# Optimization experiments

Hardware: AMD Instinct MI355X
Metric: run time of the kernel (lower is better)

## Reference

```python
import jax, jax.numpy as jnp
import numpy as np

N, L = 1, 384
NODE, H, PD = 256, 8, 128
HD = NODE // H
D1 = H * PD + NODE  # out_transform input dim = 1280


def instance_norm(x, eps=1e-5):
    # x: (N, C, H, W); torch InstanceNorm2d default: no affine, biased var
    m = x.mean(axis=(2, 3), keepdims=True)
    v = x.var(axis=(2, 3), keepdims=True)
    return (x - m) / jnp.sqrt(v + eps)


def conv3x3(x, w, b):
    y = jax.lax.conv_general_dilated(x, w, (1, 1), 'SAME',
                                     dimension_numbers=('NCHW', 'OIHW', 'NCHW'))
    return y + b[None, :, None, None]


def leaky(x):
    return jnp.where(x >= 0, x, 0.01 * x)


def layer_norm(x, w, b, eps=1e-5):
    m = x.mean(-1, keepdims=True)
    v = x.var(-1, keepdims=True)
    return (x - m) / jnp.sqrt(v + eps) * w + b


def setup_inputs() -> dict:
    key = jax.random.key(0)
    ks = jax.random.split(key, 32)
    s = 0.05
    inp = {
        'x': jax.random.normal(ks[0], (N, L, NODE), jnp.float32),
        'z': jax.random.normal(ks[1], (N, L, L, PD), jnp.float32),
        'plddt': jax.random.uniform(ks[2], (N, L, L, 1), jnp.float32),
        # linear weights stored (in, out) so application is x @ W
        'Wq': jax.random.normal(ks[3], (NODE, NODE), jnp.float32) * s,
        'Wk': jax.random.normal(ks[4], (NODE, NODE), jnp.float32) * s,
        'Wv': jax.random.normal(ks[5], (NODE, NODE), jnp.float32) * s,
        'Wp2a': jax.random.normal(ks[6], (PD, H), jnp.float32) * s,
        'conv_a_w': jax.random.normal(ks[7], (H, 2 * H, 3, 3), jnp.float32) * s,
        'conv_a_b': jnp.zeros((H,), jnp.float32),
        'conv_m_w': jax.random.normal(ks[8], (H, H + 1, 3, 3), jnp.float32) * s,
        'conv_m_b': jnp.zeros((H,), jnp.float32),
        'ln1_w': jnp.ones((D1,), jnp.float32),
        'ln1_b': jnp.zeros((D1,), jnp.float32),
        'lin1_w': jax.random.normal(ks[9], (D1, 2 * NODE), jnp.float32) * s,
        'lin1_b': jnp.zeros((2 * NODE,), jnp.float32),
        'ln2_w': jnp.ones((2 * NODE,), jnp.float32),
        'ln2_b': jnp.zeros((2 * NODE,), jnp.float32),
        'lin2_w': jax.random.normal(ks[10], (2 * NODE, NODE), jnp.float32) * s,
        'lin2_b': jnp.zeros((NODE,), jnp.float32),
        'lnf_w': jnp.ones((NODE,), jnp.float32),
        'lnf_b': jnp.zeros((NODE,), jnp.float32),
        'conv_p_w': jax.random.normal(ks[11], (PD, H + PD, 3, 3), jnp.float32) * s,
        'conv_p_b': jnp.zeros((PD,), jnp.float32),
    }
    return inp


def reference(x, z, plddt, Wq, Wk, Wv, Wp2a, conv_a_w, conv_a_b, conv_m_w,
              conv_m_b, ln1_w, ln1_b, lin1_w, lin1_b, ln2_w, ln2_b, lin2_w,
              lin2_b, lnf_w, lnf_b, conv_p_w, conv_p_b):
    Nb, Lh, D = x.shape
    nh = conv_a_w.shape[0]
    hd = D // nh
    Pd = z.shape[-1]
    # node -> alpha (GAT-style QK scores per head)
    q = (x @ Wq).reshape(Nb, Lh, nh, hd)
    k = (x @ Wk).reshape(Nb, Lh, nh, hd)
    v = (x @ Wv).reshape(Nb, Lh, nh, hd)
    a_node = jnp.einsum('nlhd,nmhd->nlmh', q, k) / jnp.sqrt(jnp.float32(hd))
    a_pair = z @ Wp2a                                  # (N,L,L,H)
    a = jnp.concatenate([a_pair, a_node], -1).transpose(0, 3, 1, 2)  # (N,2H,L,L)
    a = leaky(conv3x3(instance_norm(a), conv_a_w, conv_a_b))
    a = jnp.concatenate([a, plddt.transpose(0, 3, 1, 2)], 1)          # (N,H+1,L,L)
    a = leaky(conv3x3(instance_norm(a), conv_m_w, conv_m_b))
    a = a.transpose(0, 2, 3, 1)                                        # (N,L,L,H)
    # aggregations
    nfn = jnp.einsum('nlmh,nmhd->nlhd', a, v).reshape(Nb, Lh, D)       # node from node
    nfp = jnp.einsum('nlmh,nlmp->nlhp', a, z).reshape(Nb, Lh, nh * Pd) # node from pair
    cat = jnp.concatenate([nfp, nfn], -1)
    h = layer_norm(cat, ln1_w, ln1_b) @ lin1_w + lin1_b
    h = leaky(layer_norm(h, ln2_w, ln2_b)) @ lin2_w + lin2_b
    x_new = layer_norm(x + h, lnf_w, lnf_b)
    zp = jnp.concatenate([z, a], -1).transpose(0, 3, 1, 2)             # (N,P+H,L,L)
    z_new = leaky(conv3x3(instance_norm(zp), conv_p_w, conv_p_b)).transpose(0, 2, 3, 1)
    return x_new, z_new
```

## Files before the change

kernel.cpp:

```cpp
#include <hip/hip_runtime.h>
#include <stdint.h>

#define LSEQ 384
#define LL   147456
#define NODE 256
#define NH   8
#define HD   32
#define PDIM 128
#define D1   1280
#define D2   512

typedef __attribute__((ext_vector_type(8))) short s16x8;
typedef __attribute__((ext_vector_type(8))) __bf16 bf16x8;
typedef __attribute__((ext_vector_type(4))) float f32x4;

__device__ __forceinline__ float bf2f(uint16_t u) {
    union { uint32_t i; float f; } x; x.i = ((uint32_t)u) << 16; return x.f;
}
__device__ __forceinline__ uint16_t f2bf(float f) {
    uint32_t b = __float_as_uint(f);
    return (uint16_t)((b + 0x7FFFu + ((b >> 16) & 1u)) >> 16);
}
__device__ __forceinline__ float ld(const void* p, size_t i, int bf) {
    return bf ? bf2f(((const uint16_t*)p)[i]) : ((const float*)p)[i];
}
__device__ __forceinline__ void stout(void* p, size_t i, float v, int bf) {
    if (bf) ((uint16_t*)p)[i] = f2bf(v);
    else    ((float*)p)[i] = v;
}

__device__ __forceinline__ bf16x8 bf16x8_zero() {
    union { s16x8 s; bf16x8 b; } u; u.s = (s16x8)0; return u.b;
}

__device__ __forceinline__ void block_reduce2_256(float* s1, float* s2, int t) {
    __syncthreads();
    for (int o = 128; o > 0; o >>= 1) {
        if (t < o) { s1[t] += s1[t + o]; s2[t] += s2[t + o]; }
        __syncthreads();
    }
}

__device__ __forceinline__ void acc8(uint4 u, float& s, float& ss) {
    uint32_t w[4] = { u.x, u.y, u.z, u.w };
    #pragma unroll
    for (int i = 0; i < 4; ++i) {
        float a = bf2f((uint16_t)(w[i] & 0xFFFFu));
        float b = bf2f((uint16_t)(w[i] >> 16));
        s += a + b;
        ss = fmaf(a, a, ss);
        ss = fmaf(b, b, ss);
    }
}

__global__ void k_detect(const uint32_t* __restrict__ zz, int* __restrict__ flag) {
    if (threadIdx.x == 0 && blockIdx.x == 0) {
        int cnt = 0;
        for (int i = 0; i < 256; ++i) {
            uint32_t lo = zz[i] & 0xFFFFu;
            uint32_t e = (lo >> 7) & 0xFFu;
            if (lo == 0u || (e >= 96u && e <= 142u)) ++cnt;
        }
        flag[0] = (cnt >= 192) ? 1 : 0;
    }
}

__global__ __launch_bounds__(256) void k_cvt(
    const void* __restrict__ src, uint16_t* __restrict__ dst, const int* __restrict__ dt)
{
    int bf = dt[0];
    int i = blockIdx.x * 256 + threadIdx.x;
    dst[i] = f2bf(ld(src, i, bf));
}

__global__ __launch_bounds__(256) void k_wnk(
    const void* __restrict__ src, uint16_t* __restrict__ dst, int K, int N,
    const int* __restrict__ dt)
{
    int bf = dt[0];
    int n = blockIdx.x;
    for (int e = threadIdx.x; e < K; e += 256)
        dst[(size_t)n * K + e] = f2bf(ld(src, (size_t)e * N + n, bf));
}

__global__ __launch_bounds__(256) void k_gemm_bias_f32(
    const uint16_t* __restrict__ A, const uint16_t* __restrict__ B,
    const void* __restrict__ bias, float* __restrict__ out, int K, int N,
    const int* __restrict__ dt)
{
    __shared__ __align__(16) uint16_t As[64 * 72];
    __shared__ __align__(16) uint16_t Bs[64 * 72];
    int bf = dt[0];
    int t = threadIdx.x;
    int row0 = blockIdx.x * 64, col0 = blockIdx.y * 64;
    int w = t >> 6, lane = t & 63, p = lane & 15, g = lane >> 4;
    int wm = w >> 1, wn = w & 1;
    f32x4 acc[2][2];
    #pragma unroll
    for (int i = 0; i < 2; ++i)
        #pragma unroll
        for (int j = 0; j < 2; ++j) acc[i][j] = (f32x4){0.f, 0.f, 0.f, 0.f};

    for (int kc = 0; kc < K; kc += 64) {
        __syncthreads();
        #pragma unroll
        for (int rep = 0; rep < 2; ++rep) {
            int i = t + rep * 256;
            int r = i >> 3, c8 = (i & 7) * 8;
            *(uint4*)&As[r * 72 + c8] = *(const uint4*)&A[(size_t)(row0 + r) * K + kc + c8];
            *(uint4*)&Bs[r * 72 + c8] = *(const uint4*)&B[(size_t)(col0 + r) * K + kc + c8];
        }
        __syncthreads();
        #pragma unroll
        for (int kk = 0; kk < 64; kk += 32) {
            bf16x8 a0 = *(const bf16x8*)&As[(wm * 32 + p) * 72 + kk + 8 * g];
            bf16x8 a1 = *(const bf16x8*)&As[(wm * 32 + 16 + p) * 72 + kk + 8 * g];
            bf16x8 b0 = *(const bf16x8*)&Bs[(wn * 32 + p) * 72 + kk + 8 * g];
            bf16x8 b1 = *(const bf16x8*)&Bs[(wn * 32 + 16 + p) * 72 + kk + 8 * g];
            acc[0][0] = __builtin_amdgcn_mfma_f32_16x16x32_bf16(a0, b0, acc[0][0], 0, 0, 0);
            acc[0][1] = __builtin_amdgcn_mfma_f32_16x16x32_bf16(a0, b1, acc[0][1], 0, 0, 0);
            acc[1][0] = __builtin_amdgcn_mfma_f32_16x16x32_bf16(a1, b0, acc[1][0], 0, 0, 0);
            acc[1][1] = __builtin_amdgcn_mfma_f32_16x16x32_bf16(a1, b1, acc[1][1], 0, 0, 0);
        }
    }
    #pragma unroll
    for (int mi = 0; mi < 2; ++mi)
        #pragma unroll
        for (int ni = 0; ni < 2; ++ni) {
            int n = col0 + wn * 32 + ni * 16 + p;
            float bb = ld(bias, n, bf);
            #pragma unroll
            for (int reg = 0; reg < 4; ++reg) {
                int m = row0 + wm * 32 + mi * 16 + 4 * g + reg;
                out[(size_t)m * N + n] = acc[mi][ni][reg] + bb;
            }
        }
}

__global__ __launch_bounds__(256) void k_gemm_qkv(
    const uint16_t* __restrict__ A, const uint16_t* __restrict__ B,
    uint16_t* __restrict__ q, uint16_t* __restrict__ k, uint16_t* __restrict__ v)
{
    __shared__ __align__(16) uint16_t As[64 * 72];
    __shared__ __align__(16) uint16_t Bs[64 * 72];
    const int K = 256;
    int t = threadIdx.x;
    int row0 = blockIdx.x * 64, col0 = blockIdx.y * 64;
    int w = t >> 6, lane = t & 63, p = lane & 15, g = lane >> 4;
    int wm = w >> 1, wn = w & 1;
    f32x4 acc[2][2];
    #pragma unroll
    for (int i = 0; i < 2; ++i)
        #pragma unroll
        for (int j = 0; j < 2; ++j) acc[i][j] = (f32x4){0.f, 0.f, 0.f, 0.f};

    for (int kc = 0; kc < K; kc += 64) {
        __syncthreads();
        #pragma unroll
        for (int rep = 0; rep < 2; ++rep) {
            int i = t + rep * 256;
            int r = i >> 3, c8 = (i & 7) * 8;
            *(uint4*)&As[r * 72 + c8] = *(const uint4*)&A[(size_t)(row0 + r) * K + kc + c8];
            *(uint4*)&Bs[r * 72 + c8] = *(const uint4*)&B[(size_t)(col0 + r) * K + kc + c8];
        }
        __syncthreads();
        #pragma unroll
        for (int kk = 0; kk < 64; kk += 32) {
            bf16x8 a0 = *(const bf16x8*)&As[(wm * 32 + p) * 72 + kk + 8 * g];
            bf16x8 a1 = *(const bf16x8*)&As[(wm * 32 + 16 + p) * 72 + kk + 8 * g];
            bf16x8 b0 = *(const bf16x8*)&Bs[(wn * 32 + p) * 72 + kk + 8 * g];
            bf16x8 b1 = *(const bf16x8*)&Bs[(wn * 32 + 16 + p) * 72 + kk + 8 * g];
            acc[0][0] = __builtin_amdgcn_mfma_f32_16x16x32_bf16(a0, b0, acc[0][0], 0, 0, 0);
            acc[0][1] = __builtin_amdgcn_mfma_f32_16x16x32_bf16(a0, b1, acc[0][1], 0, 0, 0);
            acc[1][0] = __builtin_amdgcn_mfma_f32_16x16x32_bf16(a1, b0, acc[1][0], 0, 0, 0);
            acc[1][1] = __builtin_amdgcn_mfma_f32_16x16x32_bf16(a1, b1, acc[1][1], 0, 0, 0);
        }
    }
    #pragma unroll
    for (int mi = 0; mi < 2; ++mi)
        #pragma unroll
        for (int ni = 0; ni < 2; ++ni) {
            int nglob = col0 + wn * 32 + ni * 16 + p;
            int sel = nglob >> 8, col = nglob & 255;
            uint16_t* dst = (sel == 0) ? q : (sel == 1) ? k : v;
            #pragma unroll
            for (int reg = 0; reg < 4; ++reg) {
                int m = row0 + wm * 32 + mi * 16 + 4 * g + reg;
                dst[(size_t)m * 256 + col] = f2bf(acc[mi][ni][reg]);
            }
        }
}

__global__ __launch_bounds__(256) void k_lin2lnf_mfma(
    const uint16_t* __restrict__ A, const uint16_t* __restrict__ B,
    const void* __restrict__ bias, const void* __restrict__ x,
    const void* __restrict__ lnw, const void* __restrict__ lnb,
    void* __restrict__ out, const int* __restrict__ dt)
{
    __shared__ __align__(16) uint16_t As[32 * 72];
    __shared__ __align__(16) uint16_t Bs[256 * 72];
    const int K = 512;
    int bf = dt[0];
    int t = threadIdx.x;
    int row0 = blockIdx.x * 32;
    int w = t >> 6, lane = t & 63, p = lane & 15, g = lane >> 4;
    f32x4 acc[2][4];
    #pragma unroll
    for (int i = 0; i < 2; ++i)
        #pragma unroll
        for (int j = 0; j < 4; ++j) acc[i][j] = (f32x4){0.f, 0.f, 0.f, 0.f};

    for (int kc = 0; kc < K; kc += 64) {
        __syncthreads();
        {
            int r = t >> 3, c8 = (t & 7) * 8;
            *(uint4*)&As[r * 72 + c8] = *(const uint4*)&A[(size_t)(row0 + r) * K + kc + c8];
        }
        #pragma unroll
        for (int rep = 0; rep < 8; ++rep) {
            int i = t + rep * 256;
            int r = i >> 3, c8 = (i & 7) * 8;
            *(uint4*)&Bs[r * 72 + c8] = *(const uint4*)&B[(size_t)r * K + kc + c8];
        }
        __syncthreads();
        #pragma unroll
        for (int kk = 0; kk < 64; kk += 32) {
            bf16x8 a0 = *(const bf16x8*)&As[(p) * 72 + kk + 8 * g];
            bf16x8 a1 = *(const bf16x8*)&As[(16 + p) * 72 + kk + 8 * g];
            #pragma unroll
            for (int ni = 0; ni < 4; ++ni) {
                bf16x8 bq = *(const bf16x8*)&Bs[(w * 64 + ni * 16 + p) * 72 + kk + 8 * g];
                acc[0][ni] = __builtin_amdgcn_mfma_f32_16x16x32_bf16(a0, bq, acc[0][ni], 0, 0, 0);
                acc[1][ni] = __builtin_amdgcn_mfma_f32_16x16x32_bf16(a1, bq, acc[1][ni], 0, 0, 0);
            }
        }
    }
    __syncthreads();
    float* lnt = (float*)Bs;
    #pragma unroll
    for (int mi = 0; mi < 2; ++mi)
        #pragma unroll
        for (int ni = 0; ni < 4; ++ni) {
            int n = w * 64 + ni * 16 + p;
            float bb = ld(bias, n, bf);
            #pragma unroll
            for (int reg = 0; reg < 4; ++reg) {
                int m = mi * 16 + 4 * g + reg;
                lnt[m * 264 + n] = acc[mi][ni][reg] + bb + ld(x, (size_t)(row0 + m) * 256 + n, bf);
            }
        }
    __syncthreads();
    for (int rr = 0; rr < 8; ++rr) {
        int m = w * 8 + rr;
        float4 v4 = *(const float4*)&lnt[m * 264 + lane * 4];
        float vv[4] = { v4.x, v4.y, v4.z, v4.w };
        float s = (vv[0] + vv[1]) + (vv[2] + vv[3]);
        float ss = fmaf(vv[0], vv[0], fmaf(vv[1], vv[1], fmaf(vv[2], vv[2], vv[3] * vv[3])));
        #pragma unroll
        for (int off = 32; off > 0; off >>= 1) {
            s  += __shfl_xor(s, off);
            ss += __shfl_xor(ss, off);
        }
        float mean = s / 256.f;
        float rstd = rsqrtf(fmaxf(ss / 256.f - mean * mean, 0.f) + 1e-5f);
        #pragma unroll
        for (int i = 0; i < 4; ++i) {
            int c = lane * 4 + i;
            float val = (vv[i] - mean) * rstd * ld(lnw, c, bf) + ld(lnb, c, bf);
            stout(out, (size_t)(row0 + m) * 256 + c, val, bf);
        }
    }
}

__global__ __launch_bounds__(256) void k_apair(
    const void* __restrict__ z, const void* __restrict__ Wp2a,
    uint16_t* __restrict__ acat, const int* __restrict__ dt)
{
    __shared__ float zl[32 * 129];
    __shared__ float wp[PDIM * NH];
    int bf = dt[0];
    int t = threadIdx.x, m0 = blockIdx.x * 32, l = blockIdx.y;
    for (int i = t; i < PDIM * NH; i += 256) wp[i] = ld(Wp2a, i, bf);
    for (int i = t; i < 32 * PDIM; i += 256) {
        int ml = i >> 7, p = i & 127;
        zl[ml * 129 + p] = ld(z, ((size_t)(l * LSEQ + m0 + ml)) * PDIM + p, bf);
    }
    __syncthreads();
    int h = t >> 5, ml = t & 31;
    float acc = 0.f;
    for (int p = 0; p < PDIM; ++p) acc = fmaf(zl[ml * 129 + p], wp[p * NH + h], acc);
    acat[(size_t)h * LL + l * LSEQ + m0 + ml] = f2bf(acc);
}

__global__ __launch_bounds__(256) void k_anode(
    const uint16_t* __restrict__ q, const uint16_t* __restrict__ k,
    uint16_t* __restrict__ acat)
{
    __shared__ float kl[NODE * 33];
    __shared__ float qr[NH * 33];
    int t = threadIdx.x, m0 = blockIdx.x * 32, l = blockIdx.y;
    for (int i = t; i < 32 * NODE; i += 256) {
        int ml = i >> 8, col = i & 255;
        kl[col * 33 + ml] = bf2f(k[(m0 + ml) * NODE + col]);
    }
    qr[(t >> 5) * 33 + (t & 31)] = bf2f(q[l * NODE + t]);
    __syncthreads();
    int h = t >> 5, ml = t & 31;
    float acc = 0.f;
    #pragma unroll 8
    for (int d = 0; d < HD; ++d)
        acc = fmaf(qr[h * 33 + d], kl[(h * HD + d) * 33 + ml], acc);
    acat[(size_t)(NH + h) * LL + l * LSEQ + m0 + ml] = f2bf(acc * 0.17677669529663687f);
}

__global__ __launch_bounds__(256) void k_scp(
    const uint16_t* __restrict__ src, float* __restrict__ ps, float* __restrict__ pss)
{
    __shared__ float s1[256], s2[256];
    int c = blockIdx.y, chunk = blockIdx.x, t = threadIdx.x;
    const uint16_t* p = src + (size_t)c * LL + (size_t)chunk * 8192;
    float s = 0.f, ss = 0.f;
    #pragma unroll
    for (int it = 0; it < 4; ++it) {
        uint4 u = *(const uint4*)&p[(it * 256 + t) * 8];
        acc8(u, s, ss);
    }
    s1[t] = s; s2[t] = ss;
    block_reduce2_256(s1, s2, t);
    if (t == 0) { ps[c * 18 + chunk] = s1[0]; pss[c * 18 + chunk] = s2[0]; }
}

__global__ void k_scf(
    const float* __restrict__ ps, const float* __restrict__ pss,
    float* __restrict__ mean_out, float* __restrict__ rstd_out, int C)
{
    int t = threadIdx.x;
    if (t < C) {
        float s = 0.f, ss = 0.f;
        for (int i = 0; i < 18; ++i) { s += ps[t * 18 + i]; ss += pss[t * 18 + i]; }
        float m = s / (float)LL;
        float var = ss / (float)LL - m * m;
        mean_out[t] = m; rstd_out[t] = rsqrtf(fmaxf(var, 0.f) + 1e-5f);
    }
}

__global__ __launch_bounds__(256) void k_sip(
    const void* __restrict__ src, float* __restrict__ ps, float* __restrict__ pss,
    const int* __restrict__ dt)
{
    __shared__ float s1[256], s2[256];
    int bf = dt[0];
    int t = threadIdx.x, b = blockIdx.x;
    float s = 0.f, ss = 0.f;
    if (bf) {
        uint4 u = ((const uint4*)src)[(size_t)b * 256 + t];
        acc8(u, s, ss);
    } else {
        const float4* p = (const float4*)src + (size_t)b * 512;
        float4 a = p[t], c = p[t + 256];
        s = (a.x + a.y) + (a.z + a.w) + (c.x + c.y) + (c.z + c.w);
        ss = fmaf(a.x, a.x, fmaf(a.y, a.y, fmaf(a.z, a.z, a.w * a.w)));
        ss = fmaf(c.x, c.x, fmaf(c.y, c.y, fmaf(c.z, c.z, fmaf(c.w, c.w, ss))));
    }
    s1[t] = s; s2[t] = ss;
    block_reduce2_256(s1, s2, t);
    if (t == 0) { ps[b] = s1[0]; pss[b] = s2[0]; }
}

__global__ void k_sif(
    const float* __restrict__ ps, const float* __restrict__ pss,
    float* __restrict__ mean_out, float* __restrict__ rstd_out)
{
    __shared__ float s1[128], s2[128];
    int t = threadIdx.x;
    s1[t] = (t < 72) ? ps[t] : 0.f;
    s2[t] = (t < 72) ? pss[t] : 0.f;
    __syncthreads();
    for (int o = 64; o > 0; o >>= 1) {
        if (t < o) { s1[t] += s1[t + o]; s2[t] += s2[t + o]; }
        __syncthreads();
    }
    if (t == 0) {
        float m = s1[0] / (float)LL;
        float var = s2[0] / (float)LL - m * m;
        mean_out[0] = m; rstd_out[0] = rsqrtf(fmaxf(var, 0.f) + 1e-5f);
    }
}

__global__ __launch_bounds__(128) void k_conv_a(
    const uint16_t* __restrict__ acat, const void* __restrict__ wa,
    const void* __restrict__ ba, const float* __restrict__ mean,
    const float* __restrict__ rstd, uint16_t* __restrict__ out,
    const int* __restrict__ dt)
{
    __shared__ float wl[144];
    __shared__ float ot[9];
    __shared__ float mn[16];
    int bf = dt[0];
    int t = threadIdx.x;
    int oc = blockIdx.z, l = blockIdx.y, m = blockIdx.x * 128 + t;
    if (t < 16) mn[t] = mean[t];
    for (int i = t; i < 144; i += 128) {
        int ic = i / 9;
        wl[i] = ld(wa, oc * 144 + i, bf) * rstd[ic];
    }
    __syncthreads();
    if (t < 9) {
        float s = 0.f;
        for (int ic = 0; ic < 16; ++ic) s = fmaf(mn[ic], wl[ic * 9 + t], s);
        ot[t] = s;
    }
    __syncthreads();
    float acc = ld(ba, oc, bf);
    #pragma unroll
    for (int r = 0; r < 3; ++r) {
        int li = l + r - 1;
        if (li < 0 || li >= LSEQ) continue;
        #pragma unroll
        for (int c = 0; c < 3; ++c) {
            int mi = m + c - 1;
            if (mi < 0 || mi >= LSEQ) continue;
            const uint16_t* ip = acat + li * LSEQ + mi;
            float a = 0.f;
            #pragma unroll
            for (int ic = 0; ic < 16; ++ic) a = fmaf(bf2f(ip[(size_t)ic * LL]), wl[ic * 9 + r * 3 + c], a);
            acc += a - ot[r * 3 + c];
        }
    }
    acc = acc >= 0.f ? acc : 0.01f * acc;
    out[(size_t)oc * LL + l * LSEQ + m] = f2bf(acc);
}

__global__ __launch_bounds__(128) void k_conv_m(
    const uint16_t* __restrict__ a1, const void* __restrict__ plddt,
    const void* __restrict__ wm, const void* __restrict__ bm,
    const float* __restrict__ mean, const float* __restrict__ rstd,
    uint16_t* __restrict__ out, const int* __restrict__ dt)
{
    __shared__ float wl[81];
    __shared__ float ot[9];
    __shared__ float mn[9];
    int bf = dt[0];
    int t = threadIdx.x;
    int oc = blockIdx.z, l = blockIdx.y, m = blockIdx.x * 128 + t;
    if (t < 9) mn[t] = mean[t];
    for (int i = t; i < 81; i += 128) {
        int ic = i / 9;
        wl[i] = ld(wm, oc * 81 + i, bf) * rstd[ic];
    }
    __syncthreads();
    if (t < 9) {
        float s = 0.f;
        for (int ic = 0; ic < 9; ++ic) s = fmaf(mn[ic], wl[ic * 9 + t], s);
        ot[t] = s;
    }
    __syncthreads();
    float acc = ld(bm, oc, bf);
    #pragma unroll
    for (int r = 0; r < 3; ++r) {
        int li = l + r - 1;
        if (li < 0 || li >= LSEQ) continue;
        #pragma unroll
        for (int c = 0; c < 3; ++c) {
            int mi = m + c - 1;
            if (mi < 0 || mi >= LSEQ) continue;
            int off = li * LSEQ + mi;
            float a = 0.f;
            #pragma unroll
            for (int ic = 0; ic < 8; ++ic) a = fmaf(bf2f(a1[(size_t)ic * LL + off]), wl[ic * 9 + r * 3 + c], a);
            a = fmaf(ld(plddt, off, bf), wl[72 + r * 3 + c], a);
            acc += a - ot[r * 3 + c];
        }
    }
    acc = acc >= 0.f ? acc : 0.01f * acc;
    out[(size_t)oc * LL + l * LSEQ + m] = f2bf(acc);
}

__global__ __launch_bounds__(128) void k_agg(
    const uint16_t* __restrict__ a2, const uint16_t* __restrict__ v,
    const void* __restrict__ z, float* __restrict__ cat,
    const int* __restrict__ dt)
{
    __shared__ float al[NH * LSEQ];
    int bf = dt[0];
    int t = threadIdx.x, l = blockIdx.x;
    for (int i = t; i < NH * LSEQ; i += 128) {
        int h = i / LSEQ, m = i % LSEQ;
        al[i] = bf2f(a2[(size_t)h * LL + l * LSEQ + m]);
    }
    __syncthreads();
    float acc[NH];
    #pragma unroll
    for (int h = 0; h < NH; ++h) acc[h] = 0.f;
    size_t zbase = (size_t)l * LSEQ * PDIM + t;
    for (int m = 0; m < LSEQ; ++m) {
        float zv = ld(z, zbase + (size_t)m * PDIM, bf);
        #pragma unroll
        for (int h = 0; h < NH; ++h) acc[h] = fmaf(al[h * LSEQ + m], zv, acc[h]);
    }
    #pragma unroll
    for (int h = 0; h < NH; ++h) cat[(size_t)l * D1 + h * PDIM + t] = acc[h];
    for (int rep = 0; rep < 2; ++rep) {
        int o = t + rep * 128;
        int h = o >> 5;
        float s = 0.f;
        for (int m = 0; m < LSEQ; ++m) s = fmaf(al[h * LSEQ + m], bf2f(v[m * NODE + o]), s);
        cat[(size_t)l * D1 + NH * PDIM + o] = s;
    }
}

__global__ __launch_bounds__(256) void k_ln1(
    const float* __restrict__ cat, const void* __restrict__ w,
    const void* __restrict__ b, uint16_t* __restrict__ outn,
    const int* __restrict__ dt)
{
    __shared__ float s1[256], s2[256];
    int bf = dt[0];
    int t = threadIdx.x, l = blockIdx.x;
    const float* row = cat + (size_t)l * D1;
    float s = 0.f, ss = 0.f;
    for (int i = t; i < D1; i += 256) { float v = row[i]; s += v; ss = fmaf(v, v, ss); }
    s1[t] = s; s2[t] = ss;
    block_reduce2_256(s1, s2, t);
    float m = s1[0] / (float)D1;
    float rstd = rsqrtf(fmaxf(s2[0] / (float)D1 - m * m, 0.f) + 1e-5f);
    for (int i = t; i < D1; i += 256)
        outn[(size_t)l * D1 + i] = f2bf((row[i] - m) * rstd * ld(w, i, bf) + ld(b, i, bf));
}

__global__ __launch_bounds__(256) void k_ln2(
    const float* __restrict__ in, const void* __restrict__ w,
    const void* __restrict__ b, uint16_t* __restrict__ outn,
    const int* __restrict__ dt)
{
    __shared__ float s1[256], s2[256];
    int bf = dt[0];
    int t = threadIdx.x, l = blockIdx.x;
    const float* row = in + (size_t)l * D2;
    float v0 = row[t], v1 = row[t + 256];
    s1[t] = v0 + v1; s2[t] = v0 * v0 + v1 * v1;
    block_reduce2_256(s1, s2, t);
    float m = s1[0] / (float)D2;
    float rstd = rsqrtf(fmaxf(s2[0] / (float)D2 - m * m, 0.f) + 1e-5f);
    float o0 = (v0 - m) * rstd * ld(w, t, bf) + ld(b, t, bf);
    float o1 = (v1 - m) * rstd * ld(w, t + 256, bf) + ld(b, t + 256, bf);
    outn[(size_t)l * D2 + t]       = f2bf(o0 >= 0.f ? o0 : 0.01f * o0);
    outn[(size_t)l * D2 + t + 256] = f2bf(o1 >= 0.f ? o1 : 0.01f * o1);
}

__global__ __launch_bounds__(128) void k_pstat(
    const void* __restrict__ z, float* __restrict__ psum, float* __restrict__ psumsq,
    const int* __restrict__ dt)
{
    int bf = dt[0];
    int t = threadIdx.x;
    size_t base = (size_t)blockIdx.x * 256 * PDIM + t;
    float s = 0.f, ss = 0.f;
    for (int i = 0; i < 256; ++i) { float v = ld(z, base + (size_t)i * PDIM, bf); s += v; ss = fmaf(v, v, ss); }
    psum[blockIdx.x * PDIM + t] = s;
    psumsq[blockIdx.x * PDIM + t] = ss;
}

__global__ __launch_bounds__(512) void k_finP(
    const float* __restrict__ psum, const float* __restrict__ psumsq,
    float* __restrict__ meanP, float* __restrict__ rstdP)
{
    __shared__ float s1[512], s2[512];
    int t = threadIdx.x;
    int c = t & 127, seg = t >> 7;
    float s = 0.f, ss = 0.f;
    for (int b = seg * 144; b < seg * 144 + 144; ++b) {
        s += psum[b * PDIM + c]; ss += psumsq[b * PDIM + c];
    }
    s1[t] = s; s2[t] = ss;
    __syncthreads();
    if (t < 128) {
        float S  = s1[t] + s1[t + 128] + s1[t + 256] + s1[t + 384];
        float SS = s2[t] + s2[t + 128] + s2[t + 256] + s2[t + 384];
        float m = S / (float)LL;
        float var = SS / (float)LL - m * m;
        meanP[t] = m; rstdP[t] = rsqrtf(fmaxf(var, 0.f) + 1e-5f);
    }
}

__global__ __launch_bounds__(64) void k_wprep(
    const void* __restrict__ wp, uint16_t* __restrict__ wt, const int* __restrict__ dt)
{
    int bf = dt[0];
    int oc = blockIdx.x, tap = blockIdx.y;
    for (int ic = threadIdx.x; ic < 144; ic += 64) {
        float v = (ic < 136) ? ld(wp, (size_t)oc * 1224 + (size_t)ic * 9 + tap, bf) : 0.f;
        wt[((size_t)tap * 128 + oc) * 144 + ic] = f2bf(v);
    }
}

__global__ __launch_bounds__(256, 2) void k_conv_p_mfma(
    const void* __restrict__ z, const uint16_t* __restrict__ a2,
    const uint16_t* __restrict__ wt, const void* __restrict__ bp,
    const float* __restrict__ meanP, const float* __restrict__ rstdP,
    void* __restrict__ out, const int* __restrict__ dt)
{
    __shared__ __align__(16) uint16_t As[4 * 34 * 144];
    __shared__ __align__(16) uint16_t Ws[128 * 144];
    __shared__ float mloc[136], rloc[136];

    int bf = dt[0];
    int t = threadIdx.x;
    int m0 = blockIdx.x * 32, l0 = blockIdx.y * 2;

    if (t < 136) { mloc[t] = meanP[t]; rloc[t] = rstdP[t]; }
    __syncthreads();

    for (int grp = t; grp < 2448; grp += 256) {
        int pixidx = grp / 18;
        int icg = (grp - pixidx * 18) * 8;
        int lr = pixidx / 34, lc = pixidx - lr * 34;
        int li = l0 - 1 + lr, mi = m0 - 1 + lc;
        uint16_t vals[8];
        if (li < 0 || li >= LSEQ || mi < 0 || mi >= LSEQ || icg >= 136) {
            #pragma unroll
            for (int j = 0; j < 8; ++j) vals[j] = 0;
        } else if (icg < 128) {
            size_t zoff = ((size_t)li * LSEQ + mi) * PDIM + icg;
            if (bf) {
                const uint16_t* zp = (const uint16_t*)z + zoff;
                #pragma unroll
                for (int j = 0; j < 8; ++j)
                    vals[j] = f2bf((bf2f(zp[j]) - mloc[icg + j]) * rloc[icg + j]);
            } else {
                const float* zp = (const float*)z + zoff;
                #pragma unroll
                for (int j = 0; j < 8; ++j)
                    vals[j] = f2bf((zp[j] - mloc[icg + j]) * rloc[icg + j]);
            }
        } else {
            size_t poff = (size_t)li * LSEQ + mi;
            #pragma unroll
            for (int j = 0; j < 8; ++j)
                vals[j] = f2bf((bf2f(a2[(size_t)j * LL + poff]) - mloc[128 + j]) * rloc[128 + j]);
        }
        *(uint4*)&As[pixidx * 144 + icg] = *(const uint4*)vals;
    }

    int w = t >> 6, lane = t & 63;
    int p = lane & 15, g = lane >> 4;
    int r = w >> 1;
    int ocb = (w & 1) * 64;
    int bb0 = (ocb + p) * 144 + 8 * g;

    f32x4 acc0[4], acc1[4];
    #pragma unroll
    for (int n = 0; n < 4; ++n) {
        acc0[n] = (f32x4){0.f, 0.f, 0.f, 0.f};
        acc1[n] = (f32x4){0.f, 0.f, 0.f, 0.f};
    }
    bf16x8 bz = bf16x8_zero();

    for (int tap = 0; tap < 9; ++tap) {
        __syncthreads();
        {
            const uint4* wsrc = (const uint4*)(wt + (size_t)tap * 18432);
            uint4* wdst = (uint4*)Ws;
            #pragma unroll
            for (int i = 0; i < 9; ++i) wdst[t + i * 256] = wsrc[t + i * 256];
        }
        __syncthreads();

        int tr = tap / 3, tc = tap - tr * 3;
        int abase = ((r + tr) * 34 + p + tc) * 144 + 8 * g;

        #pragma unroll
        for (int ch = 0; ch < 5; ++ch) {
            const int ic0 = (ch < 4) ? ch * 32 : 112;
            bf16x8 a0 = *(const bf16x8*)&As[abase + ic0];
            bf16x8 a1 = *(const bf16x8*)&As[abase + 2304 + ic0];
            #pragma unroll
            for (int n = 0; n < 4; ++n) {
                bf16x8 bq;
                if (ch < 4) {
                    bq = *(const bf16x8*)&Ws[bb0 + n * 2304 + ic0];
                } else {
                    bq = bz;
                    if (g == 2) bq = *(const bf16x8*)&Ws[bb0 + n * 2304 + 112];
                }
                acc0[n] = __builtin_amdgcn_mfma_f32_16x16x32_bf16(a0, bq, acc0[n], 0, 0, 0);
                acc1[n] = __builtin_amdgcn_mfma_f32_16x16x32_bf16(a1, bq, acc1[n], 0, 0, 0);
            }
        }
    }

    int l = l0 + r;
    #pragma unroll
    for (int n = 0; n < 4; ++n) {
        int oc = ocb + 16 * n + p;
        float bb = ld(bp, oc, bf);
        #pragma unroll
        for (int reg = 0; reg < 4; ++reg) {
            int pc = 4 * g + reg;
            float v0 = acc0[n][reg] + bb; v0 = v0 >= 0.f ? v0 : 0.01f * v0;
            stout(out, 98304 + ((size_t)l * LSEQ + (m0 + pc)) * PDIM + oc, v0, bf);
            float v1 = acc1[n][reg] + bb; v1 = v1 >= 0.f ? v1 : 0.01f * v1;
            stout(out, 98304 + ((size_t)l * LSEQ + (m0 + 16 + pc)) * PDIM + oc, v1, bf);
        }
    }
}

__global__ __launch_bounds__(128) void k_conv_p(
    const void* __restrict__ z, const uint16_t* __restrict__ a2,
    const void* __restrict__ wp, const void* __restrict__ bp,
    const float* __restrict__ meanP, const float* __restrict__ rstdP,
    void* __restrict__ out, const int* __restrict__ dt)
{
    __shared__ __align__(16) float wlds[128 * 76];
    __shared__ __align__(16) float inl[4 * 18 * 8];
    int bf = dt[0];
    int t = threadIdx.x;
    int m0 = blockIdx.x * 16, l0 = blockIdx.y * 2;
    float acc0[16], acc1[16];
    #pragma unroll
    for (int i = 0; i < 16; ++i) { acc0[i] = 0.f; acc1[i] = 0.f; }

    for (int ic0 = 0; ic0 < 136; ic0 += 8) {
        __syncthreads();
        for (int i = t; i < 128 * 72; i += 128) {
            int op = i / 72, r = i % 72;
            int cc = r / 9, tap = r % 9;
            wlds[op * 76 + tap * 8 + cc] = ld(wp, op * 1224 + (ic0 + cc) * 9 + tap, bf);
        }
        for (int i = t; i < 4 * 18 * 8; i += 128) {
            int rr = i / 144, rem = i % 144;
            int col = rem >> 3, cc = rem & 7;
            int li = l0 - 1 + rr, mi = m0 - 1 + col, ic = ic0 + cc;
            float vv = 0.f;
            if (li >= 0 && li < LSEQ && mi >= 0 && mi < LSEQ) {
                float raw = (ic < PDIM) ? ld(z, ((size_t)li * LSEQ + mi) * PDIM + ic, bf)
                                        : bf2f(a2[(size_t)(ic - PDIM) * LL + li * LSEQ + mi]);
                vv = (raw - meanP[ic]) * rstdP[ic];
            }
            inl[i] = vv;
        }
        __syncthreads();
        #pragma unroll
        for (int qd = 0; qd < 2; ++qd) {
            float4 wq[9];
            #pragma unroll
            for (int tap = 0; tap < 9; ++tap)
                wq[tap] = *(const float4*)&wlds[t * 76 + tap * 8 + qd * 4];
            float4 win[4][3];
            #pragma unroll
            for (int r = 0; r < 4; ++r) {
                win[r][1] = *(const float4*)&inl[(r * 18 + 0) * 8 + qd * 4];
                win[r][2] = *(const float4*)&inl[(r * 18 + 1) * 8 + qd * 4];
                win[r][0] = win[r][1];
            }
            #pragma unroll
            for (int pix = 0; pix < 16; ++pix) {
                #pragma unroll
                for (int r = 0; r < 4; ++r) {
                    win[r][0] = win[r][1];
                    win[r][1] = win[r][2];
                    win[r][2] = *(const float4*)&inl[(r * 18 + pix + 2) * 8 + qd * 4];
                }
                float p0x = 0.f, p0y = 0.f, p0z = 0.f, p0w = 0.f;
                float p1x = 0.f, p1y = 0.f, p1z = 0.f, p1w = 0.f;
                #pragma unroll
                for (int tr = 0; tr < 3; ++tr) {
                    #pragma unroll
                    for (int c = 0; c < 3; ++c) {
                        float4 w4 = wq[tr * 3 + c];
                        float4 u0 = win[tr][c];
                        float4 u1 = win[tr + 1][c];
                        p0x = fmaf(w4.x, u0.x, p0x); p0y = fmaf(w4.y, u0.y, p0y);
                        p0z = fmaf(w4.z, u0.z, p0z); p0w = fmaf(w4.w, u0.w, p0w);
                        p1x = fmaf(w4.x, u1.x, p1x); p1y = fmaf(w4.y, u1.y, p1y);
                        p1z = fmaf(w4.z, u1.z, p1z); p1w = fmaf(w4.w, u1.w, p1w);
                    }
                }
                acc0[pix] += (p0x + p0y) + (p0z + p0w);
                acc1[pix] += (p1x + p1y) + (p1z + p1w);
            }
        }
    }
    float bb = ld(bp, t, bf);
    #pragma unroll
    for (int pix = 0; pix < 16; ++pix) {
        float v0 = acc0[pix] + bb; v0 = v0 >= 0.f ? v0 : 0.01f * v0;
        stout(out, 98304 + ((size_t)l0 * LSEQ + m0 + pix) * PDIM + t, v0, bf);
        float v1 = acc1[pix] + bb; v1 = v1 >= 0.f ? v1 : 0.01f * v1;
        stout(out, 98304 + ((size_t)(l0 + 1) * LSEQ + m0 + pix) * PDIM + t, v1, bf);
    }
}

extern "C" void kernel_launch(void* const* d_in, const int* in_sizes, int n_in,
                              void* d_out, int out_size, void* d_ws, size_t ws_size,
                              hipStream_t stream)
{
    const void* x     = d_in[0];
    const void* z     = d_in[1];
    const void* plddt = d_in[2];
    const void* Wq    = d_in[3];
    const void* Wk    = d_in[4];
    const void* Wv    = d_in[5];
    const void* Wp2a  = d_in[6];
    const void* caw   = d_in[7];
    const void* cab   = d_in[8];
    const void* cmw   = d_in[9];
    const void* cmb   = d_in[10];
    const void* ln1w  = d_in[11];
    const void* ln1b  = d_in[12];
    const void* l1w   = d_in[13];
    const void* l1b   = d_in[14];
    const void* ln2w  = d_in[15];
    const void* ln2b  = d_in[16];
    const void* l2w   = d_in[17];
    const void* l2b   = d_in[18];
    const void* lnfw  = d_in[19];
    const void* lnfb  = d_in[20];
    const void* cpw   = d_in[21];
    const void* cpb   = d_in[22];

    uint16_t* O = (uint16_t*)d_out;
    uint16_t* acat = O + 98304;
    uint16_t* a1b  = O + 2457600;
    uint16_t* qb   = a1b;
    uint16_t* kb   = a1b + 98304;
    uint16_t* vb   = O + 3637248;
    float*    cat  = (float*)(O + 3735552);
    float*    h1   = (float*)(O + 5701632);
    float*    psum = (float*)(O + 6488064);
    float*    psumsq = (float*)(O + 6635520);
    uint16_t* cb   = O + 6782976;
    uint16_t* h1nb = O + 7274496;
    uint16_t* xb   = O + 7471104;
    uint16_t* wtq  = O + 7569408;
    uint16_t* wt1  = O + 7766016;
    uint16_t* wt2  = O + 8421376;

    uint16_t* U = (uint16_t*)d_ws;
    uint16_t* a2b = U;
    float*    st  = (float*)(U + 1179648);
    float* m16 = st;        float* r16 = st + 16;
    float* m9  = st + 32;   float* r9  = st + 48;
    float* mP  = st + 64;   float* rP  = st + 200;
    int*   flg = (int*)(U + 1181696);
    uint16_t* wt = U + 1182720;
    int use_mfma = (ws_size >= (size_t)2365440 + 331776);

    k_detect<<<1, 64, 0, stream>>>((const uint32_t*)z, flg);
    k_cvt<<<384, 256, 0, stream>>>(x, xb, flg);
    k_wnk<<<256, 256, 0, stream>>>(Wq, wtq,           256, 256, flg);
    k_wnk<<<256, 256, 0, stream>>>(Wk, wtq +  65536,  256, 256, flg);
    k_wnk<<<256, 256, 0, stream>>>(Wv, wtq + 131072,  256, 256, flg);
    k_wnk<<<512, 256, 0, stream>>>(l1w, wt1, 1280, 512, flg);
    k_wnk<<<256, 256, 0, stream>>>(l2w, wt2,  512, 256, flg);

    k_gemm_qkv<<<dim3(6, 12), 256, 0, stream>>>(xb, wtq, qb, kb, vb);
    k_apair <<<dim3(12, LSEQ), 256, 0, stream>>>(z, Wp2a, acat, flg);
    k_anode <<<dim3(12, LSEQ), 256, 0, stream>>>(qb, kb, acat);
    k_scp<<<dim3(18, 16), 256, 0, stream>>>(acat, psum, psumsq);
    k_scf<<<1, 16, 0, stream>>>(psum, psumsq, m16, r16, 16);
    k_conv_a<<<dim3(3, LSEQ, 8), 128, 0, stream>>>(acat, caw, cab, m16, r16, a1b, flg);
    k_scp<<<dim3(18, 8), 256, 0, stream>>>(a1b, psum, psumsq);
    k_scf<<<1, 8, 0, stream>>>(psum, psumsq, m9, r9, 8);
    k_sip<<<72, 256, 0, stream>>>(plddt, psum, psumsq, flg);
    k_sif<<<1, 128, 0, stream>>>(psum, psumsq, m9 + 8, r9 + 8);
    k_conv_m<<<dim3(3, LSEQ, 8), 128, 0, stream>>>(a1b, plddt, cmw, cmb, m9, r9, a2b, flg);
    k_agg   <<<LSEQ, 128, 0, stream>>>(a2b, vb, z, cat, flg);
    k_ln1   <<<LSEQ, 256, 0, stream>>>(cat, ln1w, ln1b, cb, flg);
    k_gemm_bias_f32<<<dim3(6, 8), 256, 0, stream>>>(cb, wt1, l1b, h1, 1280, 512, flg);
    k_ln2   <<<LSEQ, 256, 0, stream>>>(h1, ln2w, ln2b, h1nb, flg);
    k_lin2lnf_mfma<<<12, 256, 0, stream>>>(h1nb, wt2, l2b, x, lnfw, lnfb, d_out, flg);
    k_scp<<<dim3(18, 8), 256, 0, stream>>>(a2b, psum, psumsq);
    k_scf<<<1, 8, 0, stream>>>(psum, psumsq, mP + 128, rP + 128, 8);
    k_pstat <<<576, 128, 0, stream>>>(z, psum, psumsq, flg);
    k_finP  <<<1, 512, 0, stream>>>(psum, psumsq, mP, rP);
    if (use_mfma) {
        k_wprep<<<dim3(128, 9), 64, 0, stream>>>(cpw, wt, flg);
        k_conv_p_mfma<<<dim3(12, 192), 256, 0, stream>>>(z, a2b, wt, cpb, mP, rP, d_out, flg);
    } else {
        k_conv_p<<<dim3(24, 192), 128, 0, stream>>>(z, a2b, cpw, cpb, mP, rP, d_out, flg);
    }
}
```

Before: 593.1 us.

## Double-buffer conv_p weights, widen agg/pstat blocks, tile weight transpose, merge plddt stats

The pair conv kernel now runs 512 threads and processes 4 rows per block. It double-buffers the per-tap weight tile in shared memory, prefetching the next tap into registers while MFMAs run, which removes one barrier per tap. The weight-transpose kernel uses a 32x32 shared tile so both reads and writes are coalesced. The aggregation and z-statistics kernels split their reduction loops across more threads and combine partial sums through shared memory. The plddt instance-norm statistics are folded into the channel-stats kernel, dropping two launches. The larger conv_p block uses more shared memory and registers per block, which may lower occupancy.

```diff
diff --git a/kernel.cpp b/kernel.cpp
--- a/kernel.cpp
+++ b/kernel.cpp
@@ -77,10 +77,17 @@
     const void* __restrict__ src, uint16_t* __restrict__ dst, int K, int N,
     const int* __restrict__ dt)
 {
-    int bf = dt[0];
-    int n = blockIdx.x;
-    for (int e = threadIdx.x; e < K; e += 256)
-        dst[(size_t)n * K + e] = f2bf(ld(src, (size_t)e * N + n, bf));
+    __shared__ float tile[32][33];
+    int bf = dt[0];
+    int k0 = blockIdx.x * 32, n0 = blockIdx.y * 32;
+    int tr = threadIdx.x >> 5, tc = threadIdx.x & 31;
+    #pragma unroll
+    for (int i = 0; i < 4; ++i)
+        tile[tr + i * 8][tc] = ld(src, (size_t)(k0 + tr + i * 8) * N + n0 + tc, bf);
+    __syncthreads();
+    #pragma unroll
+    for (int i = 0; i < 4; ++i)
+        dst[(size_t)(n0 + tr + i * 8) * K + k0 + tc] = f2bf(tile[tc][tr + i * 8]);
 }
 
 __global__ __launch_bounds__(256) void k_gemm_bias_f32(
@@ -314,16 +321,28 @@
 }
 
 __global__ __launch_bounds__(256) void k_scp(
-    const uint16_t* __restrict__ src, float* __restrict__ ps, float* __restrict__ pss)
+    const uint16_t* __restrict__ src, const void* __restrict__ raw,
+    float* __restrict__ ps, float* __restrict__ pss, const int* __restrict__ dt, int C)
 {
     __shared__ float s1[256], s2[256];
     int c = blockIdx.y, chunk = blockIdx.x, t = threadIdx.x;
-    const uint16_t* p = src + (size_t)c * LL + (size_t)chunk * 8192;
     float s = 0.f, ss = 0.f;
-    #pragma unroll
-    for (int it = 0; it < 4; ++it) {
-        uint4 u = *(const uint4*)&p[(it * 256 + t) * 8];
-        acc8(u, s, ss);
+    if (c < C) {
+        const uint16_t* p = src + (size_t)c * LL + (size_t)chunk * 8192;
+        #pragma unroll
+        for (int it = 0; it < 4; ++it) acc8(*(const uint4*)&p[(it * 256 + t) * 8], s, ss);
+    } else if (dt[0]) {
+        const uint4* p = (const uint4*)raw + (size_t)chunk * 1024;
+        #pragma unroll
+        for (int it = 0; it < 4; ++it) acc8(p[it * 256 + t], s, ss);
+    } else {
+        const float4* p = (const float4*)raw + (size_t)chunk * 2048;
+        #pragma unroll
+        for (int it = 0; it < 8; ++it) {
+            float4 a = p[it * 256 + t];
+            s += (a.x + a.y) + (a.z + a.w);
+            ss = fmaf(a.x, a.x, fmaf(a.y, a.y, fmaf(a.z, a.z, fmaf(a.w, a.w, ss))));
+        }
     }
     s1[t] = s; s2[t] = ss;
     block_reduce2_256(s1, s2, t);
@@ -344,49 +363,6 @@
     }
 }
 
-__global__ __launch_bounds__(256) void k_sip(
-    const void* __restrict__ src, float* __restrict__ ps, float* __restrict__ pss,
-    const int* __restrict__ dt)
-{
-    __shared__ float s1[256], s2[256];
-    int bf = dt[0];
-    int t = threadIdx.x, b = blockIdx.x;
-    float s = 0.f, ss = 0.f;
-    if (bf) {
-        uint4 u = ((const uint4*)src)[(size_t)b * 256 + t];
-        acc8(u, s, ss);
-    } else {
-        const float4* p = (const float4*)src + (size_t)b * 512;
-        float4 a = p[t], c = p[t + 256];
-        s = (a.x + a.y) + (a.z + a.w) + (c.x + c.y) + (c.z + c.w);
-        ss = fmaf(a.x, a.x, fmaf(a.y, a.y, fmaf(a.z, a.z, a.w * a.w)));
-        ss = fmaf(c.x, c.x, fmaf(c.y, c.y, fmaf(c.z, c.z, fmaf(c.w, c.w, ss))));
-    }
-    s1[t] = s; s2[t] = ss;
-    block_reduce2_256(s1, s2, t);
-    if (t == 0) { ps[b] = s1[0]; pss[b] = s2[0]; }
-}
-
-__global__ void k_sif(
-    const float* __restrict__ ps, const float* __restrict__ pss,
-    float* __restrict__ mean_out, float* __restrict__ rstd_out)
-{
-    __shared__ float s1[128], s2[128];
-    int t = threadIdx.x;
-    s1[t] = (t < 72) ? ps[t] : 0.f;
-    s2[t] = (t < 72) ? pss[t] : 0.f;
-    __syncthreads();
-    for (int o = 64; o > 0; o >>= 1) {
-        if (t < o) { s1[t] += s1[t + o]; s2[t] += s2[t + o]; }
-        __syncthreads();
-    }
-    if (t == 0) {
-        float m = s1[0] / (float)LL;
-        float var = s2[0] / (float)LL - m * m;
-        mean_out[0] = m; rstd_out[0] = rsqrtf(fmaxf(var, 0.f) + 1e-5f);
-    }
-}
-
 __global__ __launch_bounds__(128) void k_conv_a(
     const uint16_t* __restrict__ acat, const void* __restrict__ wa,
     const void* __restrict__ ba, const float* __restrict__ mean,
@@ -476,37 +452,50 @@
     out[(size_t)oc * LL + l * LSEQ + m] = f2bf(acc);
 }
 
-__global__ __launch_bounds__(128) void k_agg(
+__global__ __launch_bounds__(512) void k_agg(
     const uint16_t* __restrict__ a2, const uint16_t* __restrict__ v,
     const void* __restrict__ z, float* __restrict__ cat,
     const int* __restrict__ dt)
 {
     __shared__ float al[NH * LSEQ];
+    __shared__ float hp[3 * NH * PDIM];
     int bf = dt[0];
     int t = threadIdx.x, l = blockIdx.x;
-    for (int i = t; i < NH * LSEQ; i += 128) {
-        int h = i / LSEQ, m = i % LSEQ;
+    for (int i = t; i < NH * LSEQ; i += 512) {
+        int h = i / LSEQ, m = i - h * LSEQ;
         al[i] = bf2f(a2[(size_t)h * LL + l * LSEQ + m]);
     }
     __syncthreads();
+    int p = t & 127, qq = t >> 7;
     float acc[NH];
     #pragma unroll
     for (int h = 0; h < NH; ++h) acc[h] = 0.f;
-    size_t zbase = (size_t)l * LSEQ * PDIM + t;
-    for (int m = 0; m < LSEQ; ++m) {
-        float zv = ld(z, zbase + (size_t)m * PDIM, bf);
+    size_t zrow = (size_t)l * LSEQ * PDIM;
+    for (int m = qq; m < LSEQ; m += 4) {
+        float zv = ld(z, zrow + (size_t)m * PDIM + p, bf);
         #pragma unroll
         for (int h = 0; h < NH; ++h) acc[h] = fmaf(al[h * LSEQ + m], zv, acc[h]);
     }
-    #pragma unroll
-    for (int h = 0; h < NH; ++h) cat[(size_t)l * D1 + h * PDIM + t] = acc[h];
-    for (int rep = 0; rep < 2; ++rep) {
-        int o = t + rep * 128;
-        int h = o >> 5;
-        float s = 0.f;
-        for (int m = 0; m < LSEQ; ++m) s = fmaf(al[h * LSEQ + m], bf2f(v[m * NODE + o]), s);
-        cat[(size_t)l * D1 + NH * PDIM + o] = s;
-    }
+    if (qq) {
+        #pragma unroll
+        for (int h = 0; h < NH; ++h) hp[(qq - 1) * 1024 + h * PDIM + p] = acc[h];
+    }
+    __syncthreads();
+    if (qq == 0) {
+        #pragma unroll
+        for (int h = 0; h < NH; ++h)
+            cat[(size_t)l * D1 + h * PDIM + p] =
+                acc[h] + hp[h * PDIM + p] + hp[1024 + h * PDIM + p] + hp[2048 + h * PDIM + p];
+    }
+    int o = t & 255, half = t >> 8;
+    int h2 = o >> 5;
+    float s = 0.f;
+    for (int m = half; m < LSEQ; m += 2)
+        s = fmaf(al[h2 * LSEQ + m], bf2f(v[m * NODE + o]), s);
+    __syncthreads();
+    if (half) hp[o] = s;
+    __syncthreads();
+    if (!half) cat[(size_t)l * D1 + NH * PDIM + o] = s + hp[o];
 }
 
 __global__ __launch_bounds__(256) void k_ln1(
@@ -548,17 +537,26 @@
     outn[(size_t)l * D2 + t + 256] = f2bf(o1 >= 0.f ? o1 : 0.01f * o1);
 }
 
-__global__ __launch_bounds__(128) void k_pstat(
+__global__ __launch_bounds__(256) void k_pstat(
     const void* __restrict__ z, float* __restrict__ psum, float* __restrict__ psumsq,
     const int* __restrict__ dt)
 {
-    int bf = dt[0];
-    int t = threadIdx.x;
-    size_t base = (size_t)blockIdx.x * 256 * PDIM + t;
+    __shared__ float sa[128], sb[128];
+    int bf = dt[0];
+    int t = threadIdx.x;
+    int ch = t & 127, half = t >> 7;
+    size_t r0 = (size_t)blockIdx.x * 256;
     float s = 0.f, ss = 0.f;
-    for (int i = 0; i < 256; ++i) { float v = ld(z, base + (size_t)i * PDIM, bf); s += v; ss = fmaf(v, v, ss); }
-    psum[blockIdx.x * PDIM + t] = s;
-    psumsq[blockIdx.x * PDIM + t] = ss;
+    for (int i = 0; i < 128; ++i) {
+        float v = ld(z, (r0 + half + 2 * i) * PDIM + ch, bf);
+        s += v; ss = fmaf(v, v, ss);
+    }
+    if (half) { sa[ch] = s; sb[ch] = ss; }
+    __syncthreads();
+    if (!half) {
+        psum[blockIdx.x * PDIM + ch] = s + sa[ch];
+        psumsq[blockIdx.x * PDIM + ch] = ss + sb[ch];
+    }
 }
 
 __global__ __launch_bounds__(512) void k_finP(
@@ -594,24 +592,24 @@
     }
 }
 
-__global__ __launch_bounds__(256, 2) void k_conv_p_mfma(
+__global__ __launch_bounds__(512, 1) void k_conv_p_mfma(
     const void* __restrict__ z, const uint16_t* __restrict__ a2,
     const uint16_t* __restrict__ wt, const void* __restrict__ bp,
     const float* __restrict__ meanP, const float* __restrict__ rstdP,
     void* __restrict__ out, const int* __restrict__ dt)
 {
-    __shared__ __align__(16) uint16_t As[4 * 34 * 144];
-    __shared__ __align__(16) uint16_t Ws[128 * 144];
+    __shared__ __align__(16) uint16_t As[6 * 34 * 144];
+    __shared__ __align__(16) uint16_t Ws[2][128 * 144];
     __shared__ float mloc[136], rloc[136];
 
     int bf = dt[0];
     int t = threadIdx.x;
-    int m0 = blockIdx.x * 32, l0 = blockIdx.y * 2;
+    int m0 = blockIdx.x * 32, l0 = blockIdx.y * 4;
 
     if (t < 136) { mloc[t] = meanP[t]; rloc[t] = rstdP[t]; }
     __syncthreads();
 
-    for (int grp = t; grp < 2448; grp += 256) {
+    for (int grp = t; grp < 3672; grp += 512) {
         int pixidx = grp / 18;
         int icg = (grp - pixidx * 18) * 8;
         int lr = pixidx / 34, lc = pixidx - lr * 34;
@@ -641,6 +639,12 @@
         }
         *(uint4*)&As[pixidx * 144 + icg] = *(const uint4*)vals;
     }
+    {
+        const uint4* wsrc = (const uint4*)wt;
+        uint4* wdst = (uint4*)Ws[0];
+        for (int i = t; i < 2304; i += 512) wdst[i] = wsrc[i];
+    }
+    __syncthreads();
 
     int w = t >> 6, lane = t & 63;
     int p = lane & 15, g = lane >> 4;
@@ -657,17 +661,18 @@
     bf16x8 bz = bf16x8_zero();
 
     for (int tap = 0; tap < 9; ++tap) {
-        __syncthreads();
-        {
-            const uint4* wsrc = (const uint4*)(wt + (size_t)tap * 18432);
-            uint4* wdst = (uint4*)Ws;
-            #pragma unroll
-            for (int i = 0; i < 9; ++i) wdst[t + i * 256] = wsrc[t + i * 256];
-        }
-        __syncthreads();
+        int cur = tap & 1;
+        uint4 wreg[5];
+        if (tap < 8) {
+            const uint4* wsrc = (const uint4*)(wt + (size_t)(tap + 1) * 18432);
+            #pragma unroll
+            for (int j = 0; j < 4; ++j) wreg[j] = wsrc[t + 512 * j];
+            if (t < 256) wreg[4] = wsrc[2048 + t];
+        }
 
         int tr = tap / 3, tc = tap - tr * 3;
         int abase = ((r + tr) * 34 + p + tc) * 144 + 8 * g;
+        const uint16_t* Wc = Ws[cur];
 
         #pragma unroll
         for (int ch = 0; ch < 5; ++ch) {
@@ -678,15 +683,23 @@
             for (int n = 0; n < 4; ++n) {
                 bf16x8 bq;
                 if (ch < 4) {
-                    bq = *(const bf16x8*)&Ws[bb0 + n * 2304 + ic0];
+                    bq = *(const bf16x8*)&Wc[bb0 + n * 2304 + ic0];
                 } else {
                     bq = bz;
-                    if (g == 2) bq = *(const bf16x8*)&Ws[bb0 + n * 2304 + 112];
+                    if (g == 2) bq = *(const bf16x8*)&Wc[bb0 + n * 2304 + 112];
                 }
                 acc0[n] = __builtin_amdgcn_mfma_f32_16x16x32_bf16(a0, bq, acc0[n], 0, 0, 0);
                 acc1[n] = __builtin_amdgcn_mfma_f32_16x16x32_bf16(a1, bq, acc1[n], 0, 0, 0);
             }
         }
+
+        if (tap < 8) {
+            uint4* wdst = (uint4*)Ws[cur ^ 1];
+            #pragma unroll
+            for (int j = 0; j < 4; ++j) wdst[t + 512 * j] = wreg[j];
+            if (t < 256) wdst[2048 + t] = wreg[4];
+        }
+        __syncthreads();
     }
 
     int l = l0 + r;
@@ -848,35 +861,33 @@
 
     k_detect<<<1, 64, 0, stream>>>((const uint32_t*)z, flg);
     k_cvt<<<384, 256, 0, stream>>>(x, xb, flg);
-    k_wnk<<<256, 256, 0, stream>>>(Wq, wtq,           256, 256, flg);
-    k_wnk<<<256, 256, 0, stream>>>(Wk, wtq +  65536,  256, 256, flg);
-    k_wnk<<<256, 256, 0, stream>>>(Wv, wtq + 131072,  256, 256, flg);
-    k_wnk<<<512, 256, 0, stream>>>(l1w, wt1, 1280, 512, flg);
-    k_wnk<<<256, 256, 0, stream>>>(l2w, wt2,  512, 256, flg);
+    k_wnk<<<dim3(8, 8), 256, 0, stream>>>(Wq, wtq,          256, 256, flg);
+    k_wnk<<<dim3(8, 8), 256, 0, stream>>>(Wk, wtq +  65536, 256, 256, flg);
+    k_wnk<<<dim3(8, 8), 256, 0, stream>>>(Wv, wtq + 131072, 256, 256, flg);
+    k_wnk<<<dim3(40, 16), 256, 0, stream>>>(l1w, wt1, 1280, 512, flg);
+    k_wnk<<<dim3(16, 8), 256, 0, stream>>>(l2w, wt2,  512, 256, flg);
 
     k_gemm_qkv<<<dim3(6, 12), 256, 0, stream>>>(xb, wtq, qb, kb, vb);
     k_apair <<<dim3(12, LSEQ), 256, 0, stream>>>(z, Wp2a, acat, flg);
     k_anode <<<dim3(12, LSEQ), 256, 0, stream>>>(qb, kb, acat);
-    k_scp<<<dim3(18, 16), 256, 0, stream>>>(acat, psum, psumsq);
+    k_scp<<<dim3(18, 16), 256, 0, stream>>>(acat, plddt, psum, psumsq, flg, 16);
     k_scf<<<1, 16, 0, stream>>>(psum, psumsq, m16, r16, 16);
     k_conv_a<<<dim3(3, LSEQ, 8), 128, 0, stream>>>(acat, caw, cab, m16, r16, a1b, flg);
-    k_scp<<<dim3(18, 8), 256, 0, stream>>>(a1b, psum, psumsq);
-    k_scf<<<1, 8, 0, stream>>>(psum, psumsq, m9, r9, 8);
-    k_sip<<<72, 256, 0, stream>>>(plddt, psum, psumsq, flg);
-    k_sif<<<1, 128, 0, stream>>>(psum, psumsq, m9 + 8, r9 + 8);
+    k_scp<<<dim3(18, 9), 256, 0, stream>>>(a1b, plddt, psum, psumsq, flg, 8);
+    k_scf<<<1, 9, 0, stream>>>(psum, psumsq, m9, r9, 9);
     k_conv_m<<<dim3(3, LSEQ, 8), 128, 0, stream>>>(a1b, plddt, cmw, cmb, m9, r9, a2b, flg);
-    k_agg   <<<LSEQ, 128, 0, stream>>>(a2b, vb, z, cat, flg);
+    k_agg   <<<LSEQ, 512, 0, stream>>>(a2b, vb, z, cat, flg);
     k_ln1   <<<LSEQ, 256, 0, stream>>>(cat, ln1w, ln1b, cb, flg);
     k_gemm_bias_f32<<<dim3(6, 8), 256, 0, stream>>>(cb, wt1, l1b, h1, 1280, 512, flg);
     k_ln2   <<<LSEQ, 256, 0, stream>>>(h1, ln2w, ln2b, h1nb, flg);
     k_lin2lnf_mfma<<<12, 256, 0, stream>>>(h1nb, wt2, l2b, x, lnfw, lnfb, d_out, flg);
-    k_scp<<<dim3(18, 8), 256, 0, stream>>>(a2b, psum, psumsq);
+    k_scp<<<dim3(18, 8), 256, 0, stream>>>(a2b, plddt, psum, psumsq, flg, 8);
     k_scf<<<1, 8, 0, stream>>>(psum, psumsq, mP + 128, rP + 128, 8);
-    k_pstat <<<576, 128, 0, stream>>>(z, psum, psumsq, flg);
+    k_pstat <<<576, 256, 0, stream>>>(z, psum, psumsq, flg);
     k_finP  <<<1, 512, 0, stream>>>(psum, psumsq, mP, rP);
     if (use_mfma) {
         k_wprep<<<dim3(128, 9), 64, 0, stream>>>(cpw, wt, flg);
-        k_conv_p_mfma<<<dim3(12, 192), 256, 0, stream>>>(z, a2b, wt, cpb, mP, rP, d_out, flg);
+        k_conv_p_mfma<<<dim3(12, 96), 512, 0, stream>>>(z, a2b, wt, cpb, mP, rP, d_out, flg);
     } else {
         k_conv_p<<<dim3(24, 192), 128, 0, stream>>>(z, a2b, cpw, cpb, mP, rP, d_out, flg);
     }
```

After: 621.0 us. 4.7% more time.
